# Kernel optimization log

Hardware: AMD Instinct MI355X
Metric: run time of the kernel (lower is better)

## Reference

```python
import jax, jax.numpy as jnp
import numpy as np

N_NODES = 100000
N_EDGES = 1600000
F_IN = 128
F_OUT = 128


def _spmm(edge_row, edge_col, edge_weight, X):
    # sparse [N,N] @ dense [N,F]: gather source rows, weight, scatter-add to dest rows
    msgs = edge_weight[:, None] * X[edge_col]  # [E, F]
    return jax.ops.segment_sum(msgs, edge_row, num_segments=N_NODES)


def setup_inputs() -> dict:
    key = jax.random.key(0)
    ks = jax.random.split(key, 7)
    scale = 1.0 / np.sqrt(F_IN)
    return {
        "x": jax.random.normal(ks[0], (N_NODES, F_IN), dtype=jnp.float32),
        "edge_row": jax.random.randint(ks[1], (N_EDGES,), 0, N_NODES, dtype=jnp.int32),
        "edge_col": jax.random.randint(ks[2], (N_EDGES,), 0, N_NODES, dtype=jnp.int32),
        "edge_weight": jax.random.uniform(ks[3], (N_EDGES,), dtype=jnp.float32),
        "w1": jax.random.normal(ks[4], (F_IN, F_IN), dtype=jnp.float32) * scale,
        "w2": jax.random.normal(ks[5], (F_IN, F_OUT), dtype=jnp.float32) * scale,
        "w3": jax.random.normal(ks[6], (F_OUT, F_OUT), dtype=jnp.float32) * scale,
    }


def reference(x, edge_row, edge_col, edge_weight, w1, w2, w3):
    # dropout p=0.0 (eval) -> identity
    h = jax.nn.relu(_spmm(edge_row, edge_col, edge_weight, x @ w1))
    h = jax.nn.relu(_spmm(edge_row, edge_col, edge_weight, h @ w2))
    h = jax.nn.relu(_spmm(edge_row, edge_col, edge_weight, h @ w3))
    return h
```

## Files before the change

### kernel.cpp

```cpp
#include <hip/hip_runtime.h>

#define N_NODES 100000
#define N_EDGES 1600000
#define F 128

#define SCAN_B 1024
#define SCAN_NB ((N_NODES + SCAN_B - 1) / SCAN_B)

#define NSHARD 8
#define SHARD_E (N_EDGES / NSHARD)

#define NCHUNK 256
#define CHUNK_E (N_EDGES / NCHUNK)
#define HALF_N 50000

typedef short bf16x8 __attribute__((ext_vector_type(8)));
typedef float f32x4  __attribute__((ext_vector_type(4)));

union ABFrag {
    bf16x8 v;
    unsigned short u[8];
    uint4  q;
};

__device__ __forceinline__ unsigned short f2bf(float f) {
    unsigned int u = __float_as_uint(f);
    u += 0x7fffu + ((u >> 16) & 1u);
    return (unsigned short)(u >> 16);
}
__device__ __forceinline__ float bflo(unsigned int u) {
    return __uint_as_float(u << 16);
}
__device__ __forceinline__ float bfhi(unsigned int u) {
    return __uint_as_float(u & 0xFFFF0000u);
}

__device__ __forceinline__ void gather_accum(
    const unsigned short* __restrict__ Xb,
    const unsigned int* __restrict__ pairs,
    int beg, int end, int l16, float (&a)[8]) {
    int i = beg;
    for (; i + 3 < end; i += 4) {
        const unsigned int p0 = pairs[i], p1 = pairs[i + 1];
        const unsigned int p2 = pairs[i + 2], p3 = pairs[i + 3];
        const uint4 v0 = *(const uint4*)(Xb + (size_t)(p0 >> 15) * F + l16 * 8);
        const uint4 v1 = *(const uint4*)(Xb + (size_t)(p1 >> 15) * F + l16 * 8);
        const uint4 v2 = *(const uint4*)(Xb + (size_t)(p2 >> 15) * F + l16 * 8);
        const uint4 v3 = *(const uint4*)(Xb + (size_t)(p3 >> 15) * F + l16 * 8);
        const float w0 = bflo(p0 & 0x7FFFu);
        const float w1 = bflo(p1 & 0x7FFFu);
        const float w2 = bflo(p2 & 0x7FFFu);
        const float w3 = bflo(p3 & 0x7FFFu);
        a[0] += w0 * bflo(v0.x); a[1] += w0 * bfhi(v0.x);
        a[2] += w0 * bflo(v0.y); a[3] += w0 * bfhi(v0.y);
        a[4] += w0 * bflo(v0.z); a[5] += w0 * bfhi(v0.z);
        a[6] += w0 * bflo(v0.w); a[7] += w0 * bfhi(v0.w);
        a[0] += w1 * bflo(v1.x); a[1] += w1 * bfhi(v1.x);
        a[2] += w1 * bflo(v1.y); a[3] += w1 * bfhi(v1.y);
        a[4] += w1 * bflo(v1.z); a[5] += w1 * bfhi(v1.z);
        a[6] += w1 * bflo(v1.w); a[7] += w1 * bfhi(v1.w);
        a[0] += w2 * bflo(v2.x); a[1] += w2 * bfhi(v2.x);
        a[2] += w2 * bflo(v2.y); a[3] += w2 * bfhi(v2.y);
        a[4] += w2 * bflo(v2.z); a[5] += w2 * bfhi(v2.z);
        a[6] += w2 * bflo(v2.w); a[7] += w2 * bfhi(v2.w);
        a[0] += w3 * bflo(v3.x); a[1] += w3 * bfhi(v3.x);
        a[2] += w3 * bflo(v3.y); a[3] += w3 * bfhi(v3.y);
        a[4] += w3 * bflo(v3.z); a[5] += w3 * bfhi(v3.z);
        a[6] += w3 * bflo(v3.w); a[7] += w3 * bfhi(v3.w);
    }
    for (; i < end; ++i) {
        const unsigned int p0 = pairs[i];
        const uint4 v0 = *(const uint4*)(Xb + (size_t)(p0 >> 15) * F + l16 * 8);
        const float w0 = bflo(p0 & 0x7FFFu);
        a[0] += w0 * bflo(v0.x); a[1] += w0 * bfhi(v0.x);
        a[2] += w0 * bflo(v0.y); a[3] += w0 * bfhi(v0.y);
        a[4] += w0 * bflo(v0.z); a[5] += w0 * bfhi(v0.z);
        a[6] += w0 * bflo(v0.w); a[7] += w0 * bfhi(v0.w);
    }
}


__global__ __launch_bounds__(256) void chunk_hist(
    const int* __restrict__ erow, unsigned char* __restrict__ cb) {
    __shared__ unsigned int h[HALF_N / 4];
    const int c    = blockIdx.x >> 1;
    const int half = blockIdx.x & 1;
    const int t    = threadIdx.x;
    for (int i = t; i < HALF_N / 4; i += 256) h[i] = 0;
    __syncthreads();
    const int lo = half * HALF_N;
    for (int e = c * CHUNK_E + t; e < (c + 1) * CHUNK_E; e += 256) {
        const unsigned int d = (unsigned int)(erow[e] - lo);
        if (d < HALF_N) atomicAdd(&h[d >> 2], 1u << ((d & 3u) * 8u));
    }
    __syncthreads();
    unsigned int* dw = (unsigned int*)(cb + (size_t)c * N_NODES + lo);
    for (int i = t; i < HALF_N / 4; i += 256) dw[i] = h[i];
}

__global__ __launch_bounds__(256) void chunk_prefix(
    unsigned char* __restrict__ cb, int* __restrict__ counts) {
    const int t = blockIdx.x * 256 + threadIdx.x;
    if (t >= (N_NODES / 4) * 8) return;
    const int w   = t >> 3;
    const int sub = t & 7;
    const int c0  = sub * (NCHUNK / 8);
    unsigned int v[NCHUNK / 8];
    unsigned int sum = 0;
#pragma unroll
    for (int j = 0; j < NCHUNK / 8; ++j) {
        v[j] = *(const unsigned int*)(cb + (size_t)(c0 + j) * N_NODES + 4 * (size_t)w);
        sum += v[j];
    }
    unsigned int run = sum;
#pragma unroll
    for (int d = 1; d < 8; d <<= 1) {
        unsigned int tmp = __shfl_up(run, d, 8);
        if (sub >= d) run += tmp;
    }
    unsigned int acc = run - sum;
#pragma unroll
    for (int j = 0; j < NCHUNK / 8; ++j) {
        const unsigned int old = v[j];
        *(unsigned int*)(cb + (size_t)(c0 + j) * N_NODES + 4 * (size_t)w) = acc;
        acc += old;
    }
    if (sub == 7) {
        const int n = w * 4;
        counts[n + 0] = run & 255u;
        counts[n + 1] = (run >> 8) & 255u;
        counts[n + 2] = (run >> 16) & 255u;
        counts[n + 3] = run >> 24;
    }
}

__global__ void scan_block_sums(const int* __restrict__ counts, int* __restrict__ bsums) {
    __shared__ int s[SCAN_B];
    const int t = threadIdx.x;
    const int idx = blockIdx.x * SCAN_B + t;
    int v = (idx < N_NODES) ? counts[idx] : 0;
    s[t] = v;
    __syncthreads();
    for (int off = SCAN_B / 2; off > 0; off >>= 1) {
        if (t < off) s[t] += s[t + off];
        __syncthreads();
    }
    if (t == 0) bsums[blockIdx.x] = s[0];
}

__global__ void scan_bsums(const int* __restrict__ bsums, int* __restrict__ boffs) {
    __shared__ int s[128];
    const int t = threadIdx.x;
    int v = (t < SCAN_NB) ? bsums[t] : 0;
    s[t] = v;
    __syncthreads();
    for (int off = 1; off < 128; off <<= 1) {
        int u = (t >= off) ? s[t - off] : 0;
        __syncthreads();
        s[t] += u;
        __syncthreads();
    }
    if (t < SCAN_NB) boffs[t] = s[t] - v;
}

__global__ void scan_final(const int* __restrict__ counts, const int* __restrict__ boffs,
                           int* __restrict__ row_ptr) {
    __shared__ int s[SCAN_B];
    const int t = threadIdx.x;
    const int idx = blockIdx.x * SCAN_B + t;
    int v = (idx < N_NODES) ? counts[idx] : 0;
    s[t] = v;
    __syncthreads();
    for (int off = 1; off < SCAN_B; off <<= 1) {
        int u = (t >= off) ? s[t - off] : 0;
        __syncthreads();
        s[t] += u;
        __syncthreads();
    }
    if (idx < N_NODES) row_ptr[idx] = boffs[blockIdx.x] + s[t] - v;
    if (idx == 0) row_ptr[N_NODES] = N_EDGES;
}

__global__ __launch_bounds__(256) void chunk_rank(
    const int* __restrict__ erow, const int* __restrict__ ecol,
    const float* __restrict__ ew,
    const unsigned char* __restrict__ cb, const int* __restrict__ row_ptr,
    unsigned long long* __restrict__ rec) {
    __shared__ unsigned int h[HALF_N / 4];
    const int c    = blockIdx.x >> 1;
    const int half = blockIdx.x & 1;
    const int t    = threadIdx.x;
    for (int i = t; i < HALF_N / 4; i += 256) h[i] = 0;
    __syncthreads();
    const int lo = half * HALF_N;
    for (int e = c * CHUNK_E + t; e < (c + 1) * CHUNK_E; e += 256) {
        const int dst = erow[e];
        const unsigned int d = (unsigned int)(dst - lo);
        if (d < HALF_N) {
            const unsigned int old = atomicAdd(&h[d >> 2], 1u << ((d & 3u) * 8u));
            const unsigned int lrank = (old >> ((d & 3u) * 8u)) & 255u;
            const unsigned int pos = (unsigned int)row_ptr[dst]
                                   + (unsigned int)cb[(size_t)c * N_NODES + dst]
                                   + lrank;
            const unsigned int colw = ((unsigned int)ecol[e] << 15)
                                    | (unsigned int)f2bf(ew[e]);
            rec[e] = ((unsigned long long)pos << 32) | colw;
        }
    }
}

__global__ __launch_bounds__(256) void csr_fill_sharded(
    const unsigned long long* __restrict__ rec,
    unsigned int* __restrict__ pairs) {
    const int shard = blockIdx.x & (NSHARD - 1);
    const int e = (blockIdx.x >> 3) * 256 + threadIdx.x;
    const unsigned long long v = rec[e];
    const unsigned int pos = (unsigned int)(v >> 32);
    if ((unsigned int)(pos - (unsigned int)(shard * SHARD_E)) < (unsigned int)SHARD_E) {
        pairs[pos] = (unsigned int)v;
    }
}

__global__ void transpose_w_bf16(const float* __restrict__ W, unsigned short* __restrict__ Wt) {
    const int i = blockIdx.x * 256 + threadIdx.x;
    const int n = i >> 7;
    const int k = i & 127;
    Wt[i] = f2bf(W[k * F + n]);
}

__global__ __launch_bounds__(256) void gemm_mfma(
    const float* __restrict__ Xf,
    const unsigned short* __restrict__ Wt,
    unsigned short* __restrict__ Y)
{
    __shared__ unsigned short Wl[4 * 8 * 64 * 8];

    const int tid  = threadIdx.x;
    const int wave = tid >> 6;
    const int lane = tid & 63;

    for (int s = tid; s < 2048; s += 256) {
        const int ln  = s & 63;
        const int ntk = s >> 6;
        const int nt  = ntk & 7;
        const int kt  = ntk >> 3;
        const int n   = nt * 16 + (ln & 15);
        const int k   = kt * 32 + (ln >> 4) * 8;
        *(uint4*)(&Wl[s * 8]) = *(const uint4*)(Wt + n * F + k);
    }
    __syncthreads();

    const int m     = blockIdx.x * 64 + wave * 16 + (lane & 15);
    const bool mval = (m < N_NODES);
    const int kq    = (lane >> 4) * 8;

    f32x4 acc[8] = {};

#pragma unroll
    for (int kt = 0; kt < 4; ++kt) {
        ABFrag a;
        if (mval) {
            const float* p = Xf + (size_t)m * F + kt * 32 + kq;
            const float4 u0 = *(const float4*)p;
            const float4 u1 = *(const float4*)(p + 4);
            a.u[0] = f2bf(u0.x); a.u[1] = f2bf(u0.y);
            a.u[2] = f2bf(u0.z); a.u[3] = f2bf(u0.w);
            a.u[4] = f2bf(u1.x); a.u[5] = f2bf(u1.y);
            a.u[6] = f2bf(u1.z); a.u[7] = f2bf(u1.w);
        } else {
            a.q = make_uint4(0, 0, 0, 0);
        }
#pragma unroll
        for (int nt = 0; nt < 8; ++nt) {
            ABFrag b;
            b.q = *(const uint4*)(&Wl[((kt * 8 + nt) * 64 + lane) * 8]);
            acc[nt] = __builtin_amdgcn_mfma_f32_16x16x32_bf16(a.v, b.v, acc[nt], 0, 0, 0);
        }
    }

    const int rbase = blockIdx.x * 64 + wave * 16 + (lane >> 4) * 4;
    const int cbase = lane & 15;
#pragma unroll
    for (int r = 0; r < 4; ++r) {
        const int row = rbase + r;
        if (row < N_NODES) {
#pragma unroll
            for (int nt = 0; nt < 8; ++nt) {
                Y[(size_t)row * F + nt * 16 + cbase] = f2bf(acc[nt][r]);
            }
        }
    }
}

__global__ __launch_bounds__(256) void spmm_gemm_fused(
    const unsigned short* __restrict__ Xb,
    const int* __restrict__ row_ptr,
    const unsigned int* __restrict__ pairs,
    const unsigned short* __restrict__ Wt,
    unsigned short* __restrict__ Y)
{
    __shared__ unsigned short Al[16][136];

    const int tid = threadIdx.x;
    const int l16 = tid & 15;
    const int q   = tid >> 4;
    const int row = blockIdx.x * 16 + q;

    float a[8] = {};
    gather_accum(Xb, pairs, row_ptr[row], row_ptr[row + 1], l16, a);

    uint4 o;
    o.x = (unsigned int)f2bf(fmaxf(a[0], 0.f)) | ((unsigned int)f2bf(fmaxf(a[1], 0.f)) << 16);
    o.y = (unsigned int)f2bf(fmaxf(a[2], 0.f)) | ((unsigned int)f2bf(fmaxf(a[3], 0.f)) << 16);
    o.z = (unsigned int)f2bf(fmaxf(a[4], 0.f)) | ((unsigned int)f2bf(fmaxf(a[5], 0.f)) << 16);
    o.w = (unsigned int)f2bf(fmaxf(a[6], 0.f)) | ((unsigned int)f2bf(fmaxf(a[7], 0.f)) << 16);
    *(uint4*)(&Al[q][l16 * 8]) = o;
    __syncthreads();

    const int wave = tid >> 6;
    const int lane = tid & 63;
    const int kq   = (lane >> 4) * 8;
    const int arow = lane & 15;

    f32x4 acc[2] = {};
#pragma unroll
    for (int kt = 0; kt < 4; ++kt) {
        ABFrag af;
        af.q = *(const uint4*)(&Al[arow][kt * 32 + kq]);
#pragma unroll
        for (int nt = 0; nt < 2; ++nt) {
            const int n = wave * 32 + nt * 16 + (lane & 15);
            ABFrag bf_;
            bf_.q = *(const uint4*)(Wt + n * F + kt * 32 + kq);
            acc[nt] = __builtin_amdgcn_mfma_f32_16x16x32_bf16(af.v, bf_.v, acc[nt], 0, 0, 0);
        }
    }

    const int rbase = blockIdx.x * 16 + (lane >> 4) * 4;
    const int cbase = wave * 32 + (lane & 15);
#pragma unroll
    for (int nt = 0; nt < 2; ++nt) {
#pragma unroll
        for (int r = 0; r < 4; ++r) {
            Y[(size_t)(rbase + r) * F + cbase + nt * 16] = f2bf(acc[nt][r]);
        }
    }
}

__global__ __launch_bounds__(256) void spmm_csr_final(
    const unsigned short* __restrict__ Xb,
    const int* __restrict__ row_ptr,
    const unsigned int* __restrict__ pairs,
    float* __restrict__ Of) {
    const int tid = threadIdx.x;
    const int l16 = tid & 15;
    const int q   = tid >> 4;
    const int row = blockIdx.x * 16 + q;

    float a[8] = {};
    gather_accum(Xb, pairs, row_ptr[row], row_ptr[row + 1], l16, a);

    float4 o0 = {fmaxf(a[0], 0.f), fmaxf(a[1], 0.f), fmaxf(a[2], 0.f), fmaxf(a[3], 0.f)};
    float4 o1 = {fmaxf(a[4], 0.f), fmaxf(a[5], 0.f), fmaxf(a[6], 0.f), fmaxf(a[7], 0.f)};
    float* p = Of + (size_t)row * F + l16 * 8;
    *(float4*)p = o0;
    *(float4*)(p + 4) = o1;
}


extern "C" void kernel_launch(void* const* d_in, const int* in_sizes, int n_in,
                              void* d_out, int out_size, void* d_ws, size_t ws_size,
                              hipStream_t stream) {
    const float* x    = (const float*)d_in[0];
    const int*   erow = (const int*)d_in[1];
    const int*   ecol = (const int*)d_in[2];
    const float* ew   = (const float*)d_in[3];
    const float* w1   = (const float*)d_in[4];
    const float* w2   = (const float*)d_in[5];
    const float* w3   = (const float*)d_in[6];
    float* out = (float*)d_out;

    char* ws = (char*)d_ws;
    size_t off = 0;
    auto alloc = [&](size_t bytes) -> char* {
        char* p = ws + off;
        off += (bytes + 255) & ~(size_t)255;
        return p;
    };
    unsigned short* bufA = (unsigned short*)alloc((size_t)N_NODES * F * 2);
    unsigned short* bufB = (unsigned short*)alloc((size_t)N_NODES * F * 2);
    unsigned int* pairs  = (unsigned int*)alloc((size_t)N_EDGES * 4);
    int* counts  = (int*)alloc((size_t)N_NODES * sizeof(int));
    int* row_ptr = (int*)alloc(((size_t)N_NODES + 1) * sizeof(int));
    int* bsums   = (int*)alloc((size_t)SCAN_NB * sizeof(int));
    int* boffs   = (int*)alloc((size_t)SCAN_NB * sizeof(int));
    unsigned short* wt1 = (unsigned short*)alloc((size_t)F * F * 2);
    unsigned short* wt2 = (unsigned short*)alloc((size_t)F * F * 2);
    unsigned short* wt3 = (unsigned short*)alloc((size_t)F * F * 2);

    unsigned char* cb = (unsigned char*)bufA;
    unsigned long long* rec = (unsigned long long*)bufB;

    chunk_hist<<<NCHUNK * 2, 256, 0, stream>>>(erow, cb);
    chunk_prefix<<<((N_NODES / 4) * 8 + 255) / 256, 256, 0, stream>>>(cb, counts);
    scan_block_sums<<<SCAN_NB, SCAN_B, 0, stream>>>(counts, bsums);
    scan_bsums<<<1, 128, 0, stream>>>(bsums, boffs);
    scan_final<<<SCAN_NB, SCAN_B, 0, stream>>>(counts, boffs, row_ptr);
    chunk_rank<<<NCHUNK * 2, 256, 0, stream>>>(erow, ecol, ew, cb, row_ptr, rec);
    csr_fill_sharded<<<(N_EDGES / 256) * NSHARD, 256, 0, stream>>>(rec, pairs);

    transpose_w_bf16<<<64, 256, 0, stream>>>(w1, wt1);
    transpose_w_bf16<<<64, 256, 0, stream>>>(w2, wt2);
    transpose_w_bf16<<<64, 256, 0, stream>>>(w3, wt3);

    const int ggrid = (N_NODES + 63) / 64;
    const int sgrid = N_NODES / 16;

    gemm_mfma<<<ggrid, 256, 0, stream>>>(x, wt1, bufA);
    spmm_gemm_fused<<<sgrid, 256, 0, stream>>>(bufA, row_ptr, pairs, wt2, bufB);
    spmm_gemm_fused<<<sgrid, 256, 0, stream>>>(bufB, row_ptr, pairs, wt3, bufA);
    spmm_csr_final<<<sgrid, 256, 0, stream>>>(bufA, row_ptr, pairs, out);
}
```

Baseline: 438.0 us.

## Process SpMM rows in degree-sorted order to balance work per block

Builds a permutation of nodes bucketed by in-degree (descending) via a small histogram, scan and atomic scatter, then has the fused SpMM+GEMM and final SpMM kernels process rows in that order, so each block handles rows of similar length. This targets load imbalance and divergence among the 16 rows sharing a block. It also merges the three weight-transpose launches into one. The cost is four extra small kernels plus a memset, an extra indirection per row, and scattered output writes with lost row locality.

```diff
diff --git a/kernel.cpp b/kernel.cpp
--- a/kernel.cpp
+++ b/kernel.cpp
@@ -13,6 +13,8 @@
 #define NCHUNK 256
 #define CHUNK_E (N_EDGES / NCHUNK)
 #define HALF_N 50000
+
+#define NDEG 64
 
 typedef short bf16x8 __attribute__((ext_vector_type(8)));
 typedef float f32x4  __attribute__((ext_vector_type(4)));
@@ -181,6 +183,34 @@
     if (idx == 0) row_ptr[N_NODES] = N_EDGES;
 }
 
+
+__global__ __launch_bounds__(256) void deg_hist(
+    const int* __restrict__ counts, int* __restrict__ dh) {
+    __shared__ int h[NDEG];
+    const int t = threadIdx.x;
+    if (t < NDEG) h[t] = 0;
+    __syncthreads();
+    const int n = blockIdx.x * 256 + t;
+    if (n < N_NODES) atomicAdd(&h[min(counts[n], NDEG - 1)], 1);
+    __syncthreads();
+    if (t < NDEG && h[t]) atomicAdd(&dh[t], h[t]);
+}
+
+__global__ void deg_scan(const int* __restrict__ dh, int* __restrict__ dbase) {
+    if (threadIdx.x == 0) {
+        int acc = 0;
+        for (int d = NDEG - 1; d >= 0; --d) { dbase[d] = acc; acc += dh[d]; }
+    }
+}
+
+__global__ __launch_bounds__(256) void deg_scatter(
+    const int* __restrict__ counts, int* __restrict__ dbase, int* __restrict__ perm) {
+    const int n = blockIdx.x * 256 + threadIdx.x;
+    if (n >= N_NODES) return;
+    const int pos = atomicAdd(&dbase[min(counts[n], NDEG - 1)], 1);
+    perm[pos] = n;
+}
+
 __global__ __launch_bounds__(256) void chunk_rank(
     const int* __restrict__ erow, const int* __restrict__ ecol,
     const float* __restrict__ ew,
@@ -221,10 +251,18 @@
     }
 }
 
-__global__ void transpose_w_bf16(const float* __restrict__ W, unsigned short* __restrict__ Wt) {
-    const int i = blockIdx.x * 256 + threadIdx.x;
+__global__ void transpose_w_bf16(const float* __restrict__ W1,
+                                 const float* __restrict__ W2,
+                                 const float* __restrict__ W3,
+                                 unsigned short* __restrict__ Wt1,
+                                 unsigned short* __restrict__ Wt2,
+                                 unsigned short* __restrict__ Wt3) {
+    const int g = blockIdx.x >> 6;
+    const int i = (blockIdx.x & 63) * 256 + threadIdx.x;
     const int n = i >> 7;
     const int k = i & 127;
+    const float* W = (g == 0) ? W1 : (g == 1) ? W2 : W3;
+    unsigned short* Wt = (g == 0) ? Wt1 : (g == 1) ? Wt2 : Wt3;
     Wt[i] = f2bf(W[k * F + n]);
 }
 
@@ -296,15 +334,19 @@
     const unsigned short* __restrict__ Xb,
     const int* __restrict__ row_ptr,
     const unsigned int* __restrict__ pairs,
+    const int* __restrict__ perm,
     const unsigned short* __restrict__ Wt,
     unsigned short* __restrict__ Y)
 {
     __shared__ unsigned short Al[16][136];
+    __shared__ int rows[16];
 
     const int tid = threadIdx.x;
     const int l16 = tid & 15;
     const int q   = tid >> 4;
-    const int row = blockIdx.x * 16 + q;
+    if (tid < 16) rows[tid] = perm[blockIdx.x * 16 + tid];
+    __syncthreads();
+    const int row = rows[q];
 
     float a[8] = {};
     gather_accum(Xb, pairs, row_ptr[row], row_ptr[row + 1], l16, a);
@@ -336,13 +378,13 @@
         }
     }
 
-    const int rbase = blockIdx.x * 16 + (lane >> 4) * 4;
+    const int rq    = (lane >> 4) * 4;
     const int cbase = wave * 32 + (lane & 15);
 #pragma unroll
     for (int nt = 0; nt < 2; ++nt) {
 #pragma unroll
         for (int r = 0; r < 4; ++r) {
-            Y[(size_t)(rbase + r) * F + cbase + nt * 16] = f2bf(acc[nt][r]);
+            Y[(size_t)rows[rq + r] * F + cbase + nt * 16] = f2bf(acc[nt][r]);
         }
     }
 }
@@ -351,11 +393,12 @@
     const unsigned short* __restrict__ Xb,
     const int* __restrict__ row_ptr,
     const unsigned int* __restrict__ pairs,
+    const int* __restrict__ perm,
     float* __restrict__ Of) {
     const int tid = threadIdx.x;
     const int l16 = tid & 15;
     const int q   = tid >> 4;
-    const int row = blockIdx.x * 16 + q;
+    const int row = perm[blockIdx.x * 16 + q];
 
     float a[8] = {};
     gather_accum(Xb, pairs, row_ptr[row], row_ptr[row + 1], l16, a);
@@ -394,6 +437,9 @@
     int* row_ptr = (int*)alloc(((size_t)N_NODES + 1) * sizeof(int));
     int* bsums   = (int*)alloc((size_t)SCAN_NB * sizeof(int));
     int* boffs   = (int*)alloc((size_t)SCAN_NB * sizeof(int));
+    int* perm    = (int*)alloc((size_t)N_NODES * sizeof(int));
+    int* dh      = (int*)alloc((size_t)NDEG * sizeof(int));
+    int* dbase   = (int*)alloc((size_t)NDEG * sizeof(int));
     unsigned short* wt1 = (unsigned short*)alloc((size_t)F * F * 2);
     unsigned short* wt2 = (unsigned short*)alloc((size_t)F * F * 2);
     unsigned short* wt3 = (unsigned short*)alloc((size_t)F * F * 2);
@@ -409,15 +455,18 @@
     chunk_rank<<<NCHUNK * 2, 256, 0, stream>>>(erow, ecol, ew, cb, row_ptr, rec);
     csr_fill_sharded<<<(N_EDGES / 256) * NSHARD, 256, 0, stream>>>(rec, pairs);
 
-    transpose_w_bf16<<<64, 256, 0, stream>>>(w1, wt1);
-    transpose_w_bf16<<<64, 256, 0, stream>>>(w2, wt2);
-    transpose_w_bf16<<<64, 256, 0, stream>>>(w3, wt3);
+    hipMemsetAsync(dh, 0, NDEG * sizeof(int), stream);
+    deg_hist<<<(N_NODES + 255) / 256, 256, 0, stream>>>(counts, dh);
+    deg_scan<<<1, 64, 0, stream>>>(dh, dbase);
+    deg_scatter<<<(N_NODES + 255) / 256, 256, 0, stream>>>(counts, dbase, perm);
+
+    transpose_w_bf16<<<192, 256, 0, stream>>>(w1, w2, w3, wt1, wt2, wt3);
 
     const int ggrid = (N_NODES + 63) / 64;
     const int sgrid = N_NODES / 16;
 
     gemm_mfma<<<ggrid, 256, 0, stream>>>(x, wt1, bufA);
-    spmm_gemm_fused<<<sgrid, 256, 0, stream>>>(bufA, row_ptr, pairs, wt2, bufB);
-    spmm_gemm_fused<<<sgrid, 256, 0, stream>>>(bufB, row_ptr, pairs, wt3, bufA);
-    spmm_csr_final<<<sgrid, 256, 0, stream>>>(bufA, row_ptr, pairs, out);
-}
+    spmm_gemm_fused<<<sgrid, 256, 0, stream>>>(bufA, row_ptr, pairs, perm, wt2, bufB);
+    spmm_gemm_fused<<<sgrid, 256, 0, stream>>>(bufB, row_ptr, pairs, perm, wt3, bufA);
+    spmm_csr_final<<<sgrid, 256, 0, stream>>>(bufA, row_ptr, pairs, perm, out);
+}
```

Result: slower. 699.0 us (+59.6%).
